# Optimization experiments

Measured on AMD Instinct MI355X. Metric: run time of the kernel, lower is better.

## Reference

```python
import jax, jax.numpy as jnp
import numpy as np

KH, KW = 3, 3
IN_CH, OUT_CH = 16, 128
H, W_IN = 64, 64
HO, WO = H - KH + 1, W_IN - KW + 1  # 62, 62


def setup_inputs() -> dict:
    key = jax.random.key(0)
    kx, kw = jax.random.split(key)
    x = jax.random.normal(kx, (16, IN_CH, H, W_IN), dtype=jnp.float32)
    W = jax.random.normal(kw, (OUT_CH, IN_CH * (KH * KW) ** 2), dtype=jnp.float32)
    return {"x": x, "W": W}


def _unfold(x):
    # torch nn.Unfold ordering: (B, C*kh*kw, L) with channel-major, then kernel
    # positions row-major. Build (B, L, C, kd) to match transpose(1,2).view(...).
    B = x.shape[0]
    patches = jnp.stack(
        [x[:, :, i:i + HO, j:j + WO] for i in range(KH) for j in range(KW)],
        axis=2,
    )  # (B, C, kd, HO, WO)
    # -> (B, L, C, kd)
    return patches.reshape(B, IN_CH, KH * KW, HO * WO).transpose(0, 3, 1, 2)


def reference(x, W):
    B = x.shape[0]
    p = _unfold(x)  # (B, L, C, kd)
    # per-patch, per-channel self outer product: (B, L, C, kd, kd)
    outer = jnp.einsum("blci,blcj->blcij", p, p)
    feat = outer.reshape(B, HO * WO, -1)  # (B, L, C*kd*kd)
    out = jnp.einsum("blf,of->bol", feat, W)  # (B, O, L)
    # fold with (1,1) kernel == reshape to spatial grid
    return out.reshape(B, OUT_CH, HO, WO)
```

## Files before the change

### kernel.cpp

```cpp
#include <hip/hip_runtime.h>
#include <hip/hip_bf16.h>

#define BATCH 16
#define INCH 16
#define HH 64
#define WW 64
#define HO 62
#define WO 62
#define LTOT (HO * WO)
#define OUTCH 128
#define KFULL 1296
#define NTRI 45
#define NSC 8
#define KPC 96
#define TILE_N 124
#define NTILES 31
#define FROW 52
#define NFRAG (2 * NSC * 3 * 4 * 64)

typedef short bf16x8 __attribute__((ext_vector_type(8)));
typedef float f32x4 __attribute__((ext_vector_type(4)));

__device__ constexpr int TRI_A[NTRI] = {
  0,0,0,0,0,0,0,0,0, 1,1,1,1,1,1,1,1, 2,2,2,2,2,2,2,
  3,3,3,3,3,3, 4,4,4,4,4, 5,5,5,5, 6,6,6, 7,7, 8};
__device__ constexpr int TRI_B[NTRI] = {
  0,1,2,3,4,5,6,7,8, 1,2,3,4,5,6,7,8, 2,3,4,5,6,7,8,
  3,4,5,6,7,8, 4,5,6,7,8, 5,6,7,8, 6,7,8, 7,8, 8};

__device__ inline unsigned short f2bf(float x) {
  unsigned int u = __float_as_uint(x);
  unsigned int r = ((u >> 16) & 1u) + 0x7FFFu;
  return (unsigned short)((u + r) >> 16);
}
__device__ inline unsigned int pack2(float lo, float hi) {
  __hip_bfloat162 h = __float22bfloat162_rn(make_float2(lo, hi));
  return *reinterpret_cast<unsigned int*>(&h);
}

__device__ inline float wsym_at(const float* __restrict__ W, int sc, int o, int kl) {
  int half = kl >= 48 ? 1 : 0;
  int t = kl - 48 * half;
  if (t >= NTRI) return 0.f;
  int a = TRI_A[t], b = TRI_B[t];
  int c = sc * 2 + half;
  float v = W[o * KFULL + c * 81 + a * 9 + b];
  if (a != b) v += W[o * KFULL + c * 81 + b * 9 + a];
  return v;
}

__global__ void prep_wfrag(const float* __restrict__ W, unsigned short* __restrict__ Wf) {
  int idx = blockIdx.x * 256 + threadIdx.x;
  if (idx >= NFRAG) return;
  int lane = idx & 63;
  int mf = (idx >> 6) & 3;
  int rest = idx >> 8;
  int kc = rest % 3;
  int scg = rest / 3;
  int sc = scg & 7, g = scg >> 3;
  int o = g * 64 + mf * 16 + (lane & 15);
  int k0 = kc * 32 + (lane >> 4) * 8;
  unsigned short v[8];
#pragma unroll
  for (int e = 0; e < 8; ++e) v[e] = f2bf(wsym_at(W, sc, o, k0 + e));
  uint4 pk;
  pk.x = (unsigned)v[0] | ((unsigned)v[1] << 16);
  pk.y = (unsigned)v[2] | ((unsigned)v[3] << 16);
  pk.z = (unsigned)v[4] | ((unsigned)v[5] << 16);
  pk.w = (unsigned)v[6] | ((unsigned)v[7] << 16);
  *(uint4*)&Wf[(size_t)idx * 8] = pk;
}

template <bool USE_WS>
__global__ __launch_bounds__(256, 2) void conv2o_pipe(
    const float* __restrict__ X, const float* __restrict__ Wraw,
    const uint4* __restrict__ Wf, float* __restrict__ Out) {
  __shared__ float xs[INCH][4][64];
  __shared__ unsigned int Fl[2][128 * FROW];

  const int tid = threadIdx.x;
  const int blk = blockIdx.x;
  const int b = blk / NTILES;
  const int tile = blk % NTILES;
  const int y0 = tile * 2;
  const int l0 = tile * TILE_N;

  const int lane = tid & 63;
  const int wave = tid >> 6;
  const int g = wave >> 1;
  const int mbase = g * 64;
  const int nbase = (wave & 1) * 64;
  const int lr = lane & 15;
  const int lh = lane >> 4;

#pragma unroll
  for (int t = 0; t < 4; ++t) {
    int i = tid + t * 256;
    int chr = i >> 4, seg = i & 15;
    int ch = chr >> 2, r = chr & 3;
    *(float4*)&xs[ch][r][seg * 4] =
        *(const float4*)&X[((size_t)(b * INCH + ch) * HH + (y0 + r)) * WW + seg * 4];
  }

  const int q = tid & 127;
  const int half = tid >> 7;
  const int qrow = q / 62;
  const int qcol = q - qrow * 62;

  auto computeF = [&](int scn, int buf) {
    const unsigned base = q * FROW + half * 24;
    if (q < TILE_N) {
      const int ch = scn * 2 + half;
      float p[9];
#pragma unroll
      for (int di = 0; di < 3; ++di)
#pragma unroll
        for (int dj = 0; dj < 3; ++dj)
          p[di * 3 + dj] = xs[ch][qrow + di][qcol + dj];
#pragma unroll
      for (int j = 0; j < 6; ++j) {
        unsigned int d[4];
#pragma unroll
        for (int w = 0; w < 4; ++w) {
          const int m = 4 * j + w;
          float lo = (2 * m < NTRI) ? p[TRI_A[2 * m]] * p[TRI_B[2 * m]] : 0.f;
          float hi = (2 * m + 1 < NTRI) ? p[TRI_A[2 * m + 1]] * p[TRI_B[2 * m + 1]] : 0.f;
          d[w] = pack2(lo, hi);
        }
        *(uint4*)&Fl[buf][base + j * 4] = make_uint4(d[0], d[1], d[2], d[3]);
      }
    } else {
      const uint4 z = make_uint4(0u, 0u, 0u, 0u);
#pragma unroll
      for (int j = 0; j < 6; ++j) *(uint4*)&Fl[buf][base + j * 4] = z;
    }
  };

  auto loadA = [&](uint4* ap, int sc) {
    if (USE_WS) {
      const uint4* basep = Wf + (size_t)((g * NSC + sc) * 3) * 4 * 64;
#pragma unroll
      for (int f = 0; f < 12; ++f) ap[f] = basep[f * 64 + lane];
    } else {
#pragma unroll
      for (int kc = 0; kc < 3; ++kc)
#pragma unroll
        for (int mf = 0; mf < 4; ++mf) {
          const int o = mbase + mf * 16 + lr;
          const int k0 = kc * 32 + lh * 8;
          unsigned short v[8];
#pragma unroll
          for (int e = 0; e < 8; ++e) v[e] = f2bf(wsym_at(Wraw, sc, o, k0 + e));
          uint4 pk;
          pk.x = (unsigned)v[0] | ((unsigned)v[1] << 16);
          pk.y = (unsigned)v[2] | ((unsigned)v[3] << 16);
          pk.z = (unsigned)v[4] | ((unsigned)v[5] << 16);
          pk.w = (unsigned)v[6] | ((unsigned)v[7] << 16);
          ap[kc * 4 + mf] = pk;
        }
    }
  };

  __syncthreads();

  uint4 apf[2][12];
  loadA(apf[0], 0);
  computeF(0, 0);

  f32x4 acc[4][4];
#pragma unroll
  for (int mf = 0; mf < 4; ++mf)
#pragma unroll
    for (int nf = 0; nf < 4; ++nf) acc[mf][nf] = (f32x4){0.f, 0.f, 0.f, 0.f};

  __syncthreads();

#pragma unroll
  for (int sc = 0; sc < NSC; ++sc) {
    const int cur = sc & 1;
    const int nxt = cur ^ 1;
    if (sc + 1 < NSC) {
      loadA(apf[nxt], sc + 1);
      computeF(sc + 1, nxt);
    }
#pragma unroll
    for (int kc = 0; kc < 3; ++kc) {
      const int koff = kc * 16 + lh * 4;
      bf16x8 bfr[4];
#pragma unroll
      for (int nf = 0; nf < 4; ++nf)
        bfr[nf] = *(const bf16x8*)&Fl[cur][(nbase + nf * 16 + lr) * FROW + koff];
#pragma unroll
      for (int mf = 0; mf < 4; ++mf) {
        const bf16x8 af = __builtin_bit_cast(bf16x8, apf[cur][kc * 4 + mf]);
#pragma unroll
        for (int nf = 0; nf < 4; ++nf)
          acc[mf][nf] = __builtin_amdgcn_mfma_f32_16x16x32_bf16(af, bfr[nf], acc[mf][nf], 0, 0, 0);
      }
    }
    if (sc + 1 < NSC) __syncthreads();
  }

#pragma unroll
  for (int nf = 0; nf < 4; ++nf) {
    const int pos = nbase + nf * 16 + lr;
    if (pos < TILE_N) {
      const int l = l0 + pos;
#pragma unroll
      for (int mf = 0; mf < 4; ++mf) {
        const int o = mbase + mf * 16 + lh * 4;
        float* outp = &Out[((size_t)(b * OUTCH + o)) * LTOT + l];
#pragma unroll
        for (int r = 0; r < 4; ++r) outp[(size_t)r * LTOT] = acc[mf][nf][r];
      }
    }
  }
}

extern "C" void kernel_launch(void* const* d_in, const int* in_sizes, int n_in,
                              void* d_out, int out_size, void* d_ws, size_t ws_size,
                              hipStream_t stream) {
  const float* X = (const float*)d_in[0];
  const float* W = (const float*)d_in[1];
  float* Out = (float*)d_out;

  const size_t wf_bytes = (size_t)NFRAG * 16;
  const int use_ws = (ws_size >= wf_bytes) ? 1 : 0;

  if (use_ws) {
    prep_wfrag<<<(NFRAG + 255) / 256, 256, 0, stream>>>(W, (unsigned short*)d_ws);
    conv2o_pipe<true><<<BATCH * NTILES, 256, 0, stream>>>(X, W, (const uint4*)d_ws, Out);
  } else {
    conv2o_pipe<false><<<BATCH * NTILES, 256, 0, stream>>>(X, W, (const uint4*)d_ws, Out);
  }
}
```

Before: 86.74 us.

## Single-buffer feature tile with XOR swizzle to allow three blocks per CU

Replaces the double-buffered LDS feature tile and prefetched weight registers with a single buffer and a computeF→sync→MFMA→load→sync loop, raising launch bounds to 3 blocks per CU. Adds an XOR swizzle on LDS columns to reduce bank conflicts on fragment reads. The aim is lower LDS and register use for higher occupancy, at the cost of losing overlap between feature generation and MFMA and adding barriers.

```diff
diff --git a/kernel.cpp b/kernel.cpp
--- a/kernel.cpp
+++ b/kernel.cpp
@@ -12,7 +12,6 @@
 #define KFULL 1296
 #define NTRI 45
 #define NSC 8
-#define KPC 96
 #define TILE_N 124
 #define NTILES 31
 #define FROW 52
@@ -72,11 +71,11 @@
 }
 
 template <bool USE_WS>
-__global__ __launch_bounds__(256, 2) void conv2o_pipe(
+__global__ __launch_bounds__(256, 3) void conv2o_occ3(
     const float* __restrict__ X, const float* __restrict__ Wraw,
     const uint4* __restrict__ Wf, float* __restrict__ Out) {
   __shared__ float xs[INCH][4][64];
-  __shared__ unsigned int Fl[2][128 * FROW];
+  __shared__ unsigned int Fl[128 * FROW];
 
   const int tid = threadIdx.x;
   const int blk = blockIdx.x;
@@ -106,9 +105,10 @@
   const int half = tid >> 7;
   const int qrow = q / 62;
   const int qcol = q - qrow * 62;
-
-  auto computeF = [&](int scn, int buf) {
-    const unsigned base = q * FROW + half * 24;
+  const int xorw = ((q >> 3) & 3) << 2;
+
+  auto computeF = [&](int scn) {
+    const unsigned base = q * FROW;
     if (q < TILE_N) {
       const int ch = scn * 2 + half;
       float p[9];
@@ -127,12 +127,16 @@
           float hi = (2 * m + 1 < NTRI) ? p[TRI_A[2 * m + 1]] * p[TRI_B[2 * m + 1]] : 0.f;
           d[w] = pack2(lo, hi);
         }
-        *(uint4*)&Fl[buf][base + j * 4] = make_uint4(d[0], d[1], d[2], d[3]);
+        const int col = (half * 24 + j * 4) ^ xorw;
+        *(uint4*)&Fl[base + col] = make_uint4(d[0], d[1], d[2], d[3]);
       }
     } else {
       const uint4 z = make_uint4(0u, 0u, 0u, 0u);
 #pragma unroll
-      for (int j = 0; j < 6; ++j) *(uint4*)&Fl[buf][base + j * 4] = z;
+      for (int j = 0; j < 6; ++j) {
+        const int col = (half * 24 + j * 4) ^ xorw;
+        *(uint4*)&Fl[base + col] = z;
+      }
     }
   };
 
@@ -161,44 +165,46 @@
     }
   };
 
-  __syncthreads();
-
-  uint4 apf[2][12];
-  loadA(apf[0], 0);
-  computeF(0, 0);
-
   f32x4 acc[4][4];
 #pragma unroll
   for (int mf = 0; mf < 4; ++mf)
 #pragma unroll
     for (int nf = 0; nf < 4; ++nf) acc[mf][nf] = (f32x4){0.f, 0.f, 0.f, 0.f};
 
-  __syncthreads();
-
-#pragma unroll
-  for (int sc = 0; sc < NSC; ++sc) {
-    const int cur = sc & 1;
-    const int nxt = cur ^ 1;
-    if (sc + 1 < NSC) {
-      loadA(apf[nxt], sc + 1);
-      computeF(sc + 1, nxt);
-    }
+  auto mfmaStep = [&](const uint4* ap) {
 #pragma unroll
     for (int kc = 0; kc < 3; ++kc) {
       const int koff = kc * 16 + lh * 4;
       bf16x8 bfr[4];
 #pragma unroll
-      for (int nf = 0; nf < 4; ++nf)
-        bfr[nf] = *(const bf16x8*)&Fl[cur][(nbase + nf * 16 + lr) * FROW + koff];
+      for (int nf = 0; nf < 4; ++nf) {
+        const int row = nbase + nf * 16 + lr;
+        const int col = koff ^ (((row >> 3) & 3) << 2);
+        bfr[nf] = *(const bf16x8*)&Fl[row * FROW + col];
+      }
 #pragma unroll
       for (int mf = 0; mf < 4; ++mf) {
-        const bf16x8 af = __builtin_bit_cast(bf16x8, apf[cur][kc * 4 + mf]);
+        const bf16x8 af = __builtin_bit_cast(bf16x8, ap[kc * 4 + mf]);
 #pragma unroll
         for (int nf = 0; nf < 4; ++nf)
           acc[mf][nf] = __builtin_amdgcn_mfma_f32_16x16x32_bf16(af, bfr[nf], acc[mf][nf], 0, 0, 0);
       }
     }
-    if (sc + 1 < NSC) __syncthreads();
+  };
+
+  uint4 apf[12];
+  loadA(apf, 0);
+  __syncthreads();
+
+#pragma unroll 1
+  for (int sc = 0; sc < NSC; ++sc) {
+    computeF(sc);
+    __syncthreads();
+    mfmaStep(apf);
+    if (sc + 1 < NSC) {
+      loadA(apf, sc + 1);
+      __syncthreads();
+    }
   }
 
 #pragma unroll
@@ -229,8 +235,8 @@
 
   if (use_ws) {
     prep_wfrag<<<(NFRAG + 255) / 256, 256, 0, stream>>>(W, (unsigned short*)d_ws);
-    conv2o_pipe<true><<<BATCH * NTILES, 256, 0, stream>>>(X, W, (const uint4*)d_ws, Out);
+    conv2o_occ3<true><<<BATCH * NTILES, 256, 0, stream>>>(X, W, (const uint4*)d_ws, Out);
   } else {
-    conv2o_pipe<false><<<BATCH * NTILES, 256, 0, stream>>>(X, W, (const uint4*)d_ws, Out);
-  }
-}
+    conv2o_occ3<false><<<BATCH * NTILES, 256, 0, stream>>>(X, W, (const uint4*)d_ws, Out);
+  }
+}
```

Result: no change. 86.81 us (+0.1%).
